# Optimization experiments

Hardware: AMD Instinct MI355X
Metric: run time of the kernel (lower is better)

Reference implementation:

```python
import jax, jax.numpy as jnp
import numpy as np

N, E, B = 10000, 160000, 64
D, ND, ED, L = 640, 4, 8, 6
LN_EPS = 1e-5
COS_EPS = 1e-8


def _conv(x, src, dst, ea, Wq, bq, Wk, bk, Wv, bv, We, Ws, bs):
    # PyG TransformerConv, heads=1, edge features added to key and value.
    n = x.shape[0]
    d = Wq.shape[1]
    q = x @ Wq + bq                      # [N, D]
    k = x @ Wk + bk
    v = x @ Wv + bv
    e = ea @ We                          # [E, D] edge embedding
    ke = k[src] + e                      # [E, D]
    ve = v[src] + e
    score = jnp.sum(q[dst] * ke, axis=-1) * (1.0 / np.sqrt(d).astype(np.float32))
    smax = jax.lax.stop_gradient(jax.ops.segment_max(score, dst, num_segments=n))
    p = jnp.exp(score - smax[dst])
    denom = jax.ops.segment_sum(p, dst, num_segments=n)
    alpha = p / (denom[dst] + 1e-16)     # segment softmax over incoming edges
    agg = jax.ops.segment_sum(ve * alpha[:, None], dst, num_segments=n)
    return agg + x @ Ws + bs             # root/skip connection


def _graph_embed(x, ei, ea, batch, W0q, b0q, W0k, b0k, W0v, b0v, W0e, W0s, b0s,
                 Wq, bq, Wk, bk, Wv, bv, We, Ws, bs, ln_g, ln_b, Wemb, bemb):
    src, dst = ei[0], ei[1]
    h = jax.nn.relu(_conv(x, src, dst, ea, W0q, b0q, W0k, b0k, W0v, b0v, W0e, W0s, b0s))
    for l in range(L - 1):
        h = _conv(h, src, dst, ea, Wq[l], bq[l], Wk[l], bk[l], Wv[l], bv[l], We[l], Ws[l], bs[l])
        if l < L - 2:
            h = jax.nn.relu(h)
    pooled = jax.ops.segment_sum(h, batch, num_segments=B)   # global_add_pool -> [B, D]
    mu = jnp.mean(pooled, axis=-1, keepdims=True)
    var = jnp.var(pooled, axis=-1, keepdims=True)
    z = (pooled - mu) * jax.lax.rsqrt(var + LN_EPS) * ln_g + ln_b
    return jax.nn.relu(z @ Wemb + bemb)                      # [B, D]


def setup_inputs() -> dict:
    key = jax.random.key(0)
    ks = jax.random.split(key, 32)
    s = 0.05
    inp = {
        'x_i': jax.random.normal(ks[0], (N, ND), jnp.float32),
        'edge_index_i': jax.random.randint(ks[1], (2, E), 0, N, jnp.int64),
        'edge_attr_i': jax.random.normal(ks[2], (E, ED), jnp.float32),
        'batch_i': jnp.sort(jax.random.randint(ks[3], (N,), 0, B, jnp.int64)),
        'x_j': jax.random.normal(ks[4], (N, ND), jnp.float32),
        'edge_index_j': jax.random.randint(ks[5], (2, E), 0, N, jnp.int64),
        'edge_attr_j': jax.random.normal(ks[6], (E, ED), jnp.float32),
        'batch_j': jnp.sort(jax.random.randint(ks[7], (N,), 0, B, jnp.int64)),
        # layer 0 (in=node_dim)
        'W0q': jax.random.normal(ks[8], (ND, D), jnp.float32) * s,
        'b0q': jnp.zeros((D,), jnp.float32),
        'W0k': jax.random.normal(ks[9], (ND, D), jnp.float32) * s,
        'b0k': jnp.zeros((D,), jnp.float32),
        'W0v': jax.random.normal(ks[10], (ND, D), jnp.float32) * s,
        'b0v': jnp.zeros((D,), jnp.float32),
        'W0e': jax.random.normal(ks[11], (ED, D), jnp.float32) * s,
        'W0s': jax.random.normal(ks[12], (ND, D), jnp.float32) * s,
        'b0s': jnp.zeros((D,), jnp.float32),
        # layers 1..L-1 (in=out=D), stacked
        'Wq': jax.random.normal(ks[13], (L - 1, D, D), jnp.float32) * s,
        'bq': jnp.zeros((L - 1, D), jnp.float32),
        'Wk': jax.random.normal(ks[14], (L - 1, D, D), jnp.float32) * s,
        'bk': jnp.zeros((L - 1, D), jnp.float32),
        'Wv': jax.random.normal(ks[15], (L - 1, D, D), jnp.float32) * s,
        'bv': jnp.zeros((L - 1, D), jnp.float32),
        'We': jax.random.normal(ks[16], (L - 1, ED, D), jnp.float32) * s,
        'Ws': jax.random.normal(ks[17], (L - 1, D, D), jnp.float32) * s,
        'bs': jnp.zeros((L - 1, D), jnp.float32),
        # embedding head: LayerNorm + Linear + ReLU
        'ln_g': jnp.ones((D,), jnp.float32),
        'ln_b': jnp.zeros((D,), jnp.float32),
        'Wemb': jax.random.normal(ks[18], (D, D), jnp.float32) * s,
        'bemb': jnp.zeros((D,), jnp.float32),
    }
    return inp


def reference(x_i, edge_index_i, edge_attr_i, batch_i,
              x_j, edge_index_j, edge_attr_j, batch_j,
              W0q, b0q, W0k, b0k, W0v, b0v, W0e, W0s, b0s,
              Wq, bq, Wk, bk, Wv, bv, We, Ws, bs,
              ln_g, ln_b, Wemb, bemb):
    zi = _graph_embed(x_i, edge_index_i, edge_attr_i, batch_i, W0q, b0q, W0k, b0k, W0v, b0v,
                      W0e, W0s, b0s, Wq, bq, Wk, bk, Wv, bv, We, Ws, bs, ln_g, ln_b, Wemb, bemb)
    zj = _graph_embed(x_j, edge_index_j, edge_attr_j, batch_j, W0q, b0q, W0k, b0k, W0v, b0v,
                      W0e, W0s, b0s, Wq, bq, Wk, bk, Wv, bv, We, Ws, bs, ln_g, ln_b, Wemb, bemb)
    ni = jnp.maximum(jnp.linalg.norm(zi, axis=-1), COS_EPS)
    nj = jnp.maximum(jnp.linalg.norm(zj, axis=-1), COS_EPS)
    return jnp.sum(zi * zj, axis=-1) / (ni * nj)   # [B]
```

## Files before the change

kernel.cpp:

```cpp
#include <hip/hip_runtime.h>

#define N_NODES 10000
#define N_EDGES 160000
#define NB 64
#define D 640
#define ND_IN 4
#define ED_IN 8
#define NLAYERS 6
#define M_ROWS (2 * N_NODES)

#define SCORE_SCALE 0.039528470752104741f
#define NEGBIG -3.4e38f

typedef __attribute__((ext_vector_type(4))) float floatx4;
typedef __attribute__((ext_vector_type(2))) float floatx2;

__device__ __forceinline__ unsigned short f2bf(float f) {
  unsigned u = __float_as_uint(f);
  u += 0x7fffu + ((u >> 16) & 1);
  return (unsigned short)(u >> 16);
}
__device__ __forceinline__ float bf2f(unsigned short s) {
  return __uint_as_float((unsigned)s << 16);
}
__device__ __forceinline__ void gload_lds16(const void* g, void* l) {
  __builtin_amdgcn_global_load_lds(
      (const __attribute__((address_space(1))) void*)g,
      (__attribute__((address_space(3))) void*)l, 16, 0, 0);
}
__device__ __forceinline__ float4 cvt4(ushort4 s) {
  return make_float4(bf2f(s.x), bf2f(s.y), bf2f(s.z), bf2f(s.w));
}
__device__ __forceinline__ float4 fp8x4_to_f4(unsigned u) {
  floatx2 lo = __builtin_amdgcn_cvt_pk_f32_fp8((int)u, false);
  floatx2 hi = __builtin_amdgcn_cvt_pk_f32_fp8((int)u, true);
  return make_float4(lo[0], lo[1], hi[0], hi[1]);
}
__device__ __forceinline__ unsigned f4_to_fp8x4(float a, float b, float c, float d) {
  int pk = __builtin_amdgcn_cvt_pk_fp8_f32(a, b, 0, false);
  pk = __builtin_amdgcn_cvt_pk_fp8_f32(c, d, pk, true);
  return (unsigned)pk;
}
__device__ __forceinline__ unsigned char f2fp8(float a) {
  return (unsigned char)(__builtin_amdgcn_cvt_pk_fp8_f32(a, 0.f, 0, false) & 0xFF);
}

__global__ void k_lin4(const float* __restrict__ xI, const float* __restrict__ xJ,
                       const float* __restrict__ Wq, const float* __restrict__ bq,
                       const float* __restrict__ Wk, const float* __restrict__ bk,
                       const float* __restrict__ Wv, const float* __restrict__ bv,
                       const float* __restrict__ Ws, const float* __restrict__ bs,
                       unsigned short* __restrict__ oqb, unsigned char* __restrict__ okv,
                       unsigned short* __restrict__ osb) {
  int t = blockIdx.x * blockDim.x + threadIdx.x;
  if (t >= M_ROWS * D) return;
  int z = blockIdx.z;
  const float* W = (z == 0) ? Wq : (z == 1) ? Wk : (z == 2) ? Wv : Ws;
  const float* b = (z == 0) ? bq : (z == 1) ? bk : (z == 2) ? bv : bs;
  int n = t / D, d = t % D;
  const float* xr = (n < N_NODES) ? xI + (size_t)n * ND_IN
                                  : xJ + (size_t)(n - N_NODES) * ND_IN;
  float acc = b[d];
#pragma unroll
  for (int c = 0; c < ND_IN; ++c) acc += xr[c] * W[c * D + d];
  if (z == 0) oqb[t] = f2bf(acc);
  else if (z == 3) osb[t] = f2bf(acc);
  else okv[(size_t)(2 * n + (z - 1)) * D + d] = f2fp8(acc);
}

__global__ __launch_bounds__(256) void k_wprep(const float* __restrict__ Wq,
                                               const float* __restrict__ Wk,
                                               const float* __restrict__ Wv,
                                               const float* __restrict__ Ws,
                                               unsigned char* __restrict__ Wt8) {
  __shared__ float tile[32][33];
  int mt = blockIdx.z;
  int l = mt >> 2, mat = mt & 3;
  const float* W =
      (mat == 0 ? Wq : mat == 1 ? Wk : mat == 2 ? Wv : Ws) + (size_t)l * D * D;
  int tk = blockIdx.x * 32, tn = blockIdx.y * 32;
  int tx = threadIdx.x & 31, ty = threadIdx.x >> 5;
#pragma unroll
  for (int i = 0; i < 32; i += 8)
    tile[ty + i][tx] = W[(size_t)(tk + ty + i) * D + tn + tx];
  __syncthreads();
  unsigned char* dst = Wt8 + (size_t)mt * D * D;
#pragma unroll
  for (int i = 0; i < 32; i += 8)
    dst[(size_t)(tn + ty + i) * D + tk + tx] = f2fp8(tile[tx][ty + i]);
}

#define BM 128
#define BN 128
#define BKF 128
#define RBANDS ((M_ROWS + BM - 1) / BM)
__global__ __launch_bounds__(256) void k_gemm_fp8(
    const unsigned char* __restrict__ Af8, const unsigned char* __restrict__ Wt8,
    const float* __restrict__ b0, const float* __restrict__ b1,
    const float* __restrict__ b2, const float* __restrict__ b3,
    unsigned short* __restrict__ oqb, unsigned char* __restrict__ okv,
    unsigned short* __restrict__ osb) {
  __shared__ __attribute__((aligned(16))) unsigned char lA[BM * BKF];
  __shared__ __attribute__((aligned(16))) unsigned char lB[BN * BKF];
  const int f = blockIdx.x;
  const int xcd = f & 7;
  const int slot = f >> 3;
  const int grp = slot / 20;
  const int tt = slot - grp * 20;
  const int r = xcd + (grp << 3);
  if (r >= RBANDS) return;
  const int z = tt / 5;
  const int by = tt - z * 5;
  const unsigned char* Wz = Wt8 + (size_t)z * D * D;
  const float* bias = (z == 0) ? b0 : (z == 1) ? b1 : (z == 2) ? b2 : b3;
  const int bm = r * BM, bn = by * BN;
  const int t = threadIdx.x;
  const int lane = t & 63, wv = t >> 6;
  const int wm = (wv & 1) * 64, wn = (wv >> 1) * 64;
  const int l15 = lane & 15, l4 = lane >> 4;
  const int srow = lane >> 3;
  const int scb = lane & 7;

  floatx4 acc[4][4] = {};

  for (int k0 = 0; k0 < D; k0 += BKF) {
#pragma unroll
    for (int i = 0; i < 4; ++i) {
      int row = wv * 32 + i * 8 + srow;
      int lcb = scb ^ (row & 7);
      gload_lds16(Af8 + (size_t)(bm + row) * D + k0 + lcb * 16,
                  lA + (size_t)(wv * 32 + i * 8) * BKF);
      gload_lds16(Wz + (size_t)(bn + row) * D + k0 + lcb * 16,
                  lB + (size_t)(wv * 32 + i * 8) * BKF);
    }
    __syncthreads();
#pragma unroll
    for (int kk = 0; kk < 4; ++kk) {
      long af[4], bfr[4];
      int c8 = kk * 4 + l4;
      int blk = c8 >> 1, sub = (c8 & 1) * 8;
#pragma unroll
      for (int i = 0; i < 4; ++i) {
        int rowA = wm + i * 16 + l15;
        af[i] = *(const long*)(lA + (size_t)rowA * BKF +
                               (blk ^ (rowA & 7)) * 16 + sub);
        int rowB = wn + i * 16 + l15;
        bfr[i] = *(const long*)(lB + (size_t)rowB * BKF +
                                (blk ^ (rowB & 7)) * 16 + sub);
      }
#pragma unroll
      for (int ni = 0; ni < 4; ++ni)
#pragma unroll
        for (int mi = 0; mi < 4; ++mi)
          acc[ni][mi] = __builtin_amdgcn_mfma_f32_16x16x32_fp8_fp8(
              bfr[ni], af[mi], acc[ni][mi], 0, 0, 0);
    }
    __syncthreads();
  }
  float4 bia[4];
#pragma unroll
  for (int ni = 0; ni < 4; ++ni)
    bia[ni] = *(const float4*)(bias + bn + wn + ni * 16 + l4 * 4);
#pragma unroll
  for (int mi = 0; mi < 4; ++mi) {
    int row = bm + wm + mi * 16 + l15;
    if (row >= M_ROWS) continue;
#pragma unroll
    for (int ni = 0; ni < 4; ++ni) {
      int col = bn + wn + ni * 16 + l4 * 4;
      float v0 = acc[ni][mi][0] + bia[ni].x;
      float v1 = acc[ni][mi][1] + bia[ni].y;
      float v2 = acc[ni][mi][2] + bia[ni].z;
      float v3 = acc[ni][mi][3] + bia[ni].w;
      if (z == 0 || z == 3) {
        ushort4 pk;
        pk.x = f2bf(v0);
        pk.y = f2bf(v1);
        pk.z = f2bf(v2);
        pk.w = f2bf(v3);
        unsigned short* dst = (z == 0) ? oqb : osb;
        *(ushort4*)(dst + (size_t)row * D + col) = pk;
      } else {
        unsigned pk8 = f4_to_fp8x4(v0, v1, v2, v3);
        *(unsigned*)(okv + (size_t)(2 * row + (z - 1)) * D + col) = pk8;
      }
    }
  }
}

__global__ void k_hist(const int* __restrict__ dstI, const int* __restrict__ dstJ,
                       int* __restrict__ cnt) {
  int e = blockIdx.x * blockDim.x + threadIdx.x;
  if (e >= 2 * N_EDGES) return;
  int d = (e < N_EDGES) ? dstI[e] : (dstJ[e - N_EDGES] + N_NODES);
  atomicAdd(&cnt[d], 1);
}

__global__ __launch_bounds__(1024) void k_scan(const int* __restrict__ cnt,
                                               int* __restrict__ start,
                                               int* __restrict__ cursor) {
  __shared__ int sh[1024];
  __shared__ int carry_sh;
  int tid = threadIdx.x;
  if (tid == 0) {
    carry_sh = 0;
    start[0] = 0;
  }
  __syncthreads();
  for (int base = 0; base < M_ROWS; base += 1024) {
    int idx = base + tid;
    int v = (idx < M_ROWS) ? cnt[idx] : 0;
    sh[tid] = v;
    __syncthreads();
    for (int off = 1; off < 1024; off <<= 1) {
      int t = (tid >= off) ? sh[tid - off] : 0;
      __syncthreads();
      sh[tid] += t;
      __syncthreads();
    }
    int incl = sh[tid] + carry_sh;
    if (idx < M_ROWS) {
      start[idx + 1] = incl;
      cursor[idx] = incl - v;
    }
    __syncthreads();
    if (tid == 1023) carry_sh = incl;
    __syncthreads();
  }
}

__global__ void k_scatter(const int* __restrict__ srcI, const int* __restrict__ dstI,
                          const int* __restrict__ srcJ, const int* __restrict__ dstJ,
                          const float* __restrict__ eaI, const float* __restrict__ eaJ,
                          int* __restrict__ cursor, int* __restrict__ srcS,
                          float* __restrict__ eaS) {
  int e = blockIdx.x * blockDim.x + threadIdx.x;
  if (e >= 2 * N_EDGES) return;
  int s, d;
  const float* eap;
  if (e < N_EDGES) {
    s = srcI[e];
    d = dstI[e];
    eap = eaI + (size_t)e * ED_IN;
  } else {
    s = srcJ[e - N_EDGES] + N_NODES;
    d = dstJ[e - N_EDGES] + N_NODES;
    eap = eaJ + (size_t)(e - N_EDGES) * ED_IN;
  }
  int pos = atomicAdd(&cursor[d], 1);
  srcS[pos] = s;
  float4 a0 = *(const float4*)eap;
  float4 a1 = *(const float4*)(eap + 4);
  *(float4*)(eaS + (size_t)pos * ED_IN) = a0;
  *(float4*)(eaS + (size_t)pos * ED_IN + 4) = a1;
}

__global__ __launch_bounds__(256) void k_edge_fused(
    unsigned char* __restrict__ hf8, unsigned short* __restrict__ hbf,
    const unsigned short* __restrict__ sbf, const unsigned short* __restrict__ qb16,
    const unsigned char* __restrict__ kvf8, const float* __restrict__ eaS,
    const float* __restrict__ We, const int* __restrict__ srcS,
    const int* __restrict__ start, int do_relu, int write_bf) {
  int w = blockIdx.x * 4 + (threadIdx.x >> 6);
  if (w >= M_ROWS) return;
  int l64 = threadIdx.x & 63;
  int g = l64 >> 5, lane = l64 & 31;
  const int s0 = start[w], s1 = start[w + 1];
  const int deg = s1 - s0;
  const int EMAX = 2 * N_EDGES - 1;

  float4 qr[5];
#pragma unroll
  for (int i = 0; i < 5; ++i)
    qr[i] = cvt4(*(const ushort4*)(qb16 + (size_t)w * D + i * 128 + 4 * lane));

  float Gc = 0.f;
#pragma unroll
  for (int c = 0; c < ED_IN; ++c) {
    const float* wr = We + c * D;
    float p = 0.f;
#pragma unroll
    for (int i = 0; i < 5; ++i) {
      float4 wv = *(const float4*)(wr + i * 128 + 4 * lane);
      p += qr[i].x * wv.x + qr[i].y * wv.y + qr[i].z * wv.z + qr[i].w * wv.w;
    }
#pragma unroll
    for (int m = 1; m < 32; m <<= 1) p += __shfl_xor(p, m, 32);
    if (lane == c) Gc = p;
  }

  float mx = NEGBIG, Sp = 0.f, Sea = 0.f;
  float4 acc[5];
#pragma unroll
  for (int i = 0; i < 5; ++i) acc[i] = make_float4(0.f, 0.f, 0.f, 0.f);

  int p0 = s0 + g, p1 = p0 + 2;
  int c0 = min(p0, EMAX), c1 = min(p1, EMAX);
  int sj0 = srcS[c0], sj1 = srcS[c1];
  const int U = (deg + 3) >> 2;
  for (int u = 0; u < U; ++u) {
    bool ok0 = p0 < s1, ok1 = p1 < s1;
    int cc0 = c0, cc1 = c1;
    int tj0 = sj0, tj1 = sj1;
    p0 += 4;
    p1 += 4;
    c0 = min(p0, EMAX);
    c1 = min(p1, EMAX);
    sj0 = srcS[c0];
    sj1 = srcS[c1];

    const unsigned char* r0 = kvf8 + (size_t)tj0 * 2 * D;
    const unsigned char* r1 = kvf8 + (size_t)tj1 * 2 * D;
    float part0 = 0.f, part1 = 0.f;
    float4 vv0[5], vv1[5];
#pragma unroll
    for (int i = 0; i < 5; ++i) {
      int off = i * 128 + 4 * lane;
      float4 k0 = fp8x4_to_f4(*(const unsigned*)(r0 + off));
      float4 k1 = fp8x4_to_f4(*(const unsigned*)(r1 + off));
      vv0[i] = fp8x4_to_f4(*(const unsigned*)(r0 + D + off));
      vv1[i] = fp8x4_to_f4(*(const unsigned*)(r1 + D + off));
      part0 += qr[i].x * k0.x + qr[i].y * k0.y + qr[i].z * k0.z + qr[i].w * k0.w;
      part1 += qr[i].x * k1.x + qr[i].y * k1.y + qr[i].z * k1.z + qr[i].w * k1.w;
    }
    float ea0 = (lane < ED_IN) ? eaS[(size_t)cc0 * ED_IN + lane] : 0.f;
    float ea1 = (lane < ED_IN) ? eaS[(size_t)cc1 * ED_IN + lane] : 0.f;
    part0 += ea0 * Gc;
    part1 += ea1 * Gc;
#pragma unroll
    for (int m = 1; m < 32; m <<= 1) {
      part0 += __shfl_xor(part0, m, 32);
      part1 += __shfl_xor(part1, m, 32);
    }
    float sc0 = ok0 ? part0 * SCORE_SCALE : NEGBIG;
    float sc1 = ok1 ? part1 * SCORE_SCALE : NEGBIG;
    float m2 = fmaxf(sc0, sc1);
    if (m2 > mx) {
      float cs = __expf(mx - m2);
      float pA = __expf(sc0 - m2);
      float pB = __expf(sc1 - m2);
      mx = m2;
      Sp = Sp * cs + pA + pB;
      Sea = Sea * cs + pA * ea0 + pB * ea1;
#pragma unroll
      for (int i = 0; i < 5; ++i) {
        acc[i].x = acc[i].x * cs + pA * vv0[i].x + pB * vv1[i].x;
        acc[i].y = acc[i].y * cs + pA * vv0[i].y + pB * vv1[i].y;
        acc[i].z = acc[i].z * cs + pA * vv0[i].z + pB * vv1[i].z;
        acc[i].w = acc[i].w * cs + pA * vv0[i].w + pB * vv1[i].w;
      }
    } else {
      float pA = __expf(sc0 - mx);
      float pB = __expf(sc1 - mx);
      Sp += pA + pB;
      Sea += pA * ea0 + pB * ea1;
#pragma unroll
      for (int i = 0; i < 5; ++i) {
        acc[i].x += pA * vv0[i].x + pB * vv1[i].x;
        acc[i].y += pA * vv0[i].y + pB * vv1[i].y;
        acc[i].z += pA * vv0[i].z + pB * vv1[i].z;
        acc[i].w += pA * vv0[i].w + pB * vv1[i].w;
      }
    }
  }

  float mo = __shfl_xor(mx, 32);
  float mn = fmaxf(mx, mo);
  float a = __expf(mx - mn);
  float b = __expf(mo - mn);
  float Spo = __shfl_xor(Sp, 32);
  Sp = Sp * a + Spo * b;
  float Seao = __shfl_xor(Sea, 32);
  Sea = Sea * a + Seao * b;
#pragma unroll
  for (int i = 0; i < 5; ++i) {
    float ox = __shfl_xor(acc[i].x, 32);
    float oy = __shfl_xor(acc[i].y, 32);
    float oz = __shfl_xor(acc[i].z, 32);
    float ow = __shfl_xor(acc[i].w, 32);
    acc[i].x = acc[i].x * a + ox * b;
    acc[i].y = acc[i].y * a + oy * b;
    acc[i].z = acc[i].z * a + oz * b;
    acc[i].w = acc[i].w * a + ow * b;
  }
  float inv = 1.0f / (Sp + 1e-16f);
  float seac[ED_IN];
#pragma unroll
  for (int c = 0; c < ED_IN; ++c) seac[c] = __shfl(Sea, c, 32);

  for (int i = g; i < 5; i += 2) {
    int d = i * 128 + 4 * lane;
    float4 term = acc[i];
#pragma unroll
    for (int c = 0; c < ED_IN; ++c) {
      float4 wv = *(const float4*)(We + c * D + d);
      term.x += seac[c] * wv.x;
      term.y += seac[c] * wv.y;
      term.z += seac[c] * wv.z;
      term.w += seac[c] * wv.w;
    }
    ushort4 sv = *(const ushort4*)(sbf + (size_t)w * D + d);
    float vx = bf2f(sv.x) + term.x * inv;
    float vy = bf2f(sv.y) + term.y * inv;
    float vz = bf2f(sv.z) + term.z * inv;
    float vw = bf2f(sv.w) + term.w * inv;
    if (do_relu) {
      vx = fmaxf(vx, 0.f);
      vy = fmaxf(vy, 0.f);
      vz = fmaxf(vz, 0.f);
      vw = fmaxf(vw, 0.f);
    }
    if (write_bf) {
      ushort4 hb;
      hb.x = f2bf(vx);
      hb.y = f2bf(vy);
      hb.z = f2bf(vz);
      hb.w = f2bf(vw);
      *(ushort4*)(hbf + (size_t)w * D + d) = hb;
    } else {
      *(unsigned*)(hf8 + (size_t)w * D + d) = f4_to_fp8x4(vx, vy, vz, vw);
    }
  }
}

__global__ void k_ranges(const int* __restrict__ batI, const int* __restrict__ batJ,
                         int* __restrict__ rng) {
  int b = threadIdx.x;
  if (b > 2 * NB) return;
  if (b == 2 * NB) {
    rng[b] = M_ROWS;
    return;
  }
  const int* bat = (b < NB) ? batI : batJ;
  int tgt = (b < NB) ? b : b - NB;
  int lo = 0, hi = N_NODES;
  while (lo < hi) {
    int mid = (lo + hi) >> 1;
    if (bat[mid] < tgt) lo = mid + 1;
    else hi = mid;
  }
  rng[b] = lo + ((b < NB) ? 0 : N_NODES);
}

__global__ __launch_bounds__(256) void k_pool_seg(const unsigned short* __restrict__ hbf,
                                                  const int* __restrict__ rng,
                                                  float* __restrict__ pooled) {
  int b = blockIdx.x;
  int lo = rng[b], hi = rng[b + 1];
  int ch = threadIdx.x;
  if (ch >= 160) return;
  float4 s = make_float4(0.f, 0.f, 0.f, 0.f);
  for (int n = lo; n < hi; ++n) {
    ushort4 v = *(const ushort4*)(hbf + (size_t)n * D + ch * 4);
    s.x += bf2f(v.x);
    s.y += bf2f(v.y);
    s.z += bf2f(v.z);
    s.w += bf2f(v.w);
  }
  *(float4*)(pooled + (size_t)b * D + ch * 4) = s;
}

__global__ __launch_bounds__(256) void k_head(const float* __restrict__ pooled,
                                              const float* __restrict__ gam,
                                              const float* __restrict__ bet,
                                              const float* __restrict__ Wemb,
                                              const float* __restrict__ bemb,
                                              float* __restrict__ z) {
  __shared__ float sh[D];
  __shared__ float red[4];
  int b = blockIdx.x, tid = threadIdx.x;
  float local = 0.f;
  for (int c = tid; c < D; c += 256) {
    float val = pooled[(size_t)b * D + c];
    sh[c] = val;
    local += val;
  }
#pragma unroll
  for (int off = 32; off > 0; off >>= 1) local += __shfl_down(local, off);
  if ((tid & 63) == 0) red[tid >> 6] = local;
  __syncthreads();
  float mu = (red[0] + red[1] + red[2] + red[3]) * (1.0f / D);
  __syncthreads();
  float lv = 0.f;
  for (int c = tid; c < D; c += 256) {
    float t2 = sh[c] - mu;
    lv += t2 * t2;
  }
#pragma unroll
  for (int off = 32; off > 0; off >>= 1) lv += __shfl_down(lv, off);
  if ((tid & 63) == 0) red[tid >> 6] = lv;
  __syncthreads();
  float var = (red[0] + red[1] + red[2] + red[3]) * (1.0f / D);
  float rstd = rsqrtf(var + 1e-5f);
  __syncthreads();
  for (int c = tid; c < D; c += 256) sh[c] = (sh[c] - mu) * rstd * gam[c] + bet[c];
  __syncthreads();
  for (int d = tid; d < D; d += 256) {
    float acc = bemb[d];
    for (int c = 0; c < D; ++c) acc += sh[c] * Wemb[c * D + d];
    z[(size_t)b * D + d] = fmaxf(acc, 0.f);
  }
}

__global__ void k_cosine(const float* __restrict__ zi, const float* __restrict__ zj,
                         float* __restrict__ out) {
  int b = blockIdx.x, lane = threadIdx.x;
  float dot = 0.f, ni = 0.f, nj = 0.f;
  for (int d = lane; d < D; d += 64) {
    float a = zi[(size_t)b * D + d], c = zj[(size_t)b * D + d];
    dot += a * c;
    ni += a * a;
    nj += c * c;
  }
#pragma unroll
  for (int off = 32; off > 0; off >>= 1) {
    dot += __shfl_down(dot, off);
    ni += __shfl_down(ni, off);
    nj += __shfl_down(nj, off);
  }
  if (lane == 0)
    out[b] = dot / (fmaxf(sqrtf(ni), 1e-8f) * fmaxf(sqrtf(nj), 1e-8f));
}

extern "C" void kernel_launch(void* const* d_in, const int* in_sizes, int n_in,
                              void* d_out, int out_size, void* d_ws, size_t ws_size,
                              hipStream_t stream) {
  (void)in_sizes; (void)n_in; (void)out_size; (void)ws_size;
  const float* xI = (const float*)d_in[0];
  const int* eiI = (const int*)d_in[1];
  const float* eaI = (const float*)d_in[2];
  const int* batI = (const int*)d_in[3];
  const float* xJ = (const float*)d_in[4];
  const int* eiJ = (const int*)d_in[5];
  const float* eaJ = (const float*)d_in[6];
  const int* batJ = (const int*)d_in[7];
  const float* W0q = (const float*)d_in[8];
  const float* b0q = (const float*)d_in[9];
  const float* W0k = (const float*)d_in[10];
  const float* b0k = (const float*)d_in[11];
  const float* W0v = (const float*)d_in[12];
  const float* b0v = (const float*)d_in[13];
  const float* W0e = (const float*)d_in[14];
  const float* W0s = (const float*)d_in[15];
  const float* b0s = (const float*)d_in[16];
  const float* Wq = (const float*)d_in[17];
  const float* bq = (const float*)d_in[18];
  const float* Wk = (const float*)d_in[19];
  const float* bk = (const float*)d_in[20];
  const float* Wv = (const float*)d_in[21];
  const float* bv = (const float*)d_in[22];
  const float* We = (const float*)d_in[23];
  const float* Ws = (const float*)d_in[24];
  const float* bs = (const float*)d_in[25];
  const float* ln_g = (const float*)d_in[26];
  const float* ln_b = (const float*)d_in[27];
  const float* Wemb = (const float*)d_in[28];
  const float* bemb = (const float*)d_in[29];

  const size_t ND2 = (size_t)M_ROWS * D;
  float* pooled = (float*)d_ws;
  float* z = pooled + (size_t)2 * NB * D;
  float* eaS = z + (size_t)2 * NB * D;
  unsigned short* qbf = (unsigned short*)(eaS + (size_t)2 * N_EDGES * ED_IN);
  unsigned char* kvf8 = (unsigned char*)(qbf + ND2);
  unsigned char* hf8 = kvf8 + 2 * ND2;
  unsigned short* hbf = (unsigned short*)(hf8 + ND2);
  unsigned short* sbf = hbf + ND2;
  unsigned char* Wt8 = (unsigned char*)(sbf + ND2);
  int* cnt = (int*)(Wt8 + (size_t)(NLAYERS - 1) * 4 * D * D);
  int* start = cnt + M_ROWS;
  int* cursor = start + M_ROWS + 1;
  int* srcS = cursor + M_ROWS;
  int* rng = srcS + 2 * N_EDGES;

  const int* srcI = eiI;
  const int* dstI = eiI + N_EDGES;
  const int* srcJ = eiJ;
  const int* dstJ = eiJ + N_EDGES;

  dim3 gLin4((M_ROWS * D + 255) / 256, 1, 4);
  dim3 gGemm(8 * 20 * 20);
  dim3 gEdge((M_ROWS + 3) / 4);
  dim3 gE((2 * N_EDGES + 255) / 256);

  k_wprep<<<dim3(D / 32, D / 32, (NLAYERS - 1) * 4), 256, 0, stream>>>(Wq, Wk, Wv, Ws, Wt8);

  hipMemsetAsync(cnt, 0, M_ROWS * sizeof(int), stream);
  k_hist<<<gE, 256, 0, stream>>>(dstI, dstJ, cnt);
  k_scan<<<1, 1024, 0, stream>>>(cnt, start, cursor);
  k_scatter<<<gE, 256, 0, stream>>>(srcI, dstI, srcJ, dstJ, eaI, eaJ, cursor,
                                    srcS, eaS);
  k_ranges<<<1, 192, 0, stream>>>(batI, batJ, rng);

  k_lin4<<<gLin4, 256, 0, stream>>>(xI, xJ, W0q, b0q, W0k, b0k, W0v, b0v, W0s,
                                    b0s, qbf, kvf8, sbf);
  k_edge_fused<<<gEdge, 256, 0, stream>>>(hf8, hbf, sbf, qbf, kvf8, eaS, W0e,
                                          srcS, start, 1, 0);

  for (int l = 0; l < NLAYERS - 1; ++l) {
    const unsigned char* WtL = Wt8 + (size_t)l * 4 * D * D;
    const float* Wel = We + (size_t)l * ED_IN * D;
    int last = (l == NLAYERS - 2);
    k_gemm_fp8<<<gGemm, 256, 0, stream>>>(
        hf8, WtL, bq + (size_t)l * D, bk + (size_t)l * D, bv + (size_t)l * D,
        bs + (size_t)l * D, qbf, kvf8, sbf);
    k_edge_fused<<<gEdge, 256, 0, stream>>>(hf8, hbf, sbf, qbf, kvf8, eaS, Wel,
                                            srcS, start, last ? 0 : 1,
                                            last ? 1 : 0);
  }

  k_pool_seg<<<2 * NB, 256, 0, stream>>>(hbf, rng, pooled);
  k_head<<<2 * NB, 256, 0, stream>>>(pooled, ln_g, ln_b, Wemb, bemb, z);
  k_cosine<<<NB, 64, 0, stream>>>(z, z + (size_t)NB * D, (float*)d_out);
}
```

Before: 1.343 ms.

## Enlarge GEMM row tile to 256 with 8 waves; process 4 edges per half-wave in attention

The FP8 GEMM now uses 256-row tiles with 512 threads (8 waves), so each loaded weight tile is reused across twice as many rows and the grid is halved. The edge attention kernel handles four edges per half-wave iteration instead of two, issuing all K/V fp8 loads before the dot products to expose more memory-level parallelism. The edge-feature projection Gc is split across the two half-waves and merged with a shuffle. These changes raise register and LDS pressure per block and lower GEMM block count, which may reduce occupancy.

```diff
diff --git a/kernel.cpp b/kernel.cpp
--- a/kernel.cpp
+++ b/kernel.cpp
@@ -90,11 +90,11 @@
     dst[(size_t)(tn + ty + i) * D + tk + tx] = f2fp8(tile[tx][ty + i]);
 }
 
-#define BM 128
+#define BM 256
 #define BN 128
 #define BKF 128
 #define RBANDS ((M_ROWS + BM - 1) / BM)
-__global__ __launch_bounds__(256) void k_gemm_fp8(
+__global__ __launch_bounds__(512) void k_gemm_fp8(
     const unsigned char* __restrict__ Af8, const unsigned char* __restrict__ Wt8,
     const float* __restrict__ b0, const float* __restrict__ b1,
     const float* __restrict__ b2, const float* __restrict__ b3,
@@ -115,8 +115,8 @@
   const float* bias = (z == 0) ? b0 : (z == 1) ? b1 : (z == 2) ? b2 : b3;
   const int bm = r * BM, bn = by * BN;
   const int t = threadIdx.x;
-  const int lane = t & 63, wv = t >> 6;
-  const int wm = (wv & 1) * 64, wn = (wv >> 1) * 64;
+  const int lane = t & 63, wv8 = t >> 6;
+  const int wm = (wv8 & 3) * 64, wn = (wv8 >> 2) * 64;
   const int l15 = lane & 15, l4 = lane >> 4;
   const int srow = lane >> 3;
   const int scb = lane & 7;
@@ -126,12 +126,17 @@
   for (int k0 = 0; k0 < D; k0 += BKF) {
 #pragma unroll
     for (int i = 0; i < 4; ++i) {
-      int row = wv * 32 + i * 8 + srow;
+      int row = wv8 * 32 + i * 8 + srow;
       int lcb = scb ^ (row & 7);
       gload_lds16(Af8 + (size_t)(bm + row) * D + k0 + lcb * 16,
-                  lA + (size_t)(wv * 32 + i * 8) * BKF);
+                  lA + (size_t)(wv8 * 32 + i * 8) * BKF);
+    }
+#pragma unroll
+    for (int i = 0; i < 2; ++i) {
+      int row = wv8 * 16 + i * 8 + srow;
+      int lcb = scb ^ (row & 7);
       gload_lds16(Wz + (size_t)(bn + row) * D + k0 + lcb * 16,
-                  lB + (size_t)(wv * 32 + i * 8) * BKF);
+                  lB + (size_t)(wv8 * 16 + i * 8) * BKF);
     }
     __syncthreads();
 #pragma unroll
@@ -274,10 +279,10 @@
   for (int i = 0; i < 5; ++i)
     qr[i] = cvt4(*(const ushort4*)(qb16 + (size_t)w * D + i * 128 + 4 * lane));
 
-  float Gc = 0.f;
-#pragma unroll
-  for (int c = 0; c < ED_IN; ++c) {
-    const float* wr = We + c * D;
+  float gv = 0.f;
+#pragma unroll
+  for (int j = 0; j < 4; ++j) {
+    const float* wr = We + (4 * g + j) * D;
     float p = 0.f;
 #pragma unroll
     for (int i = 0; i < 5; ++i) {
@@ -286,7 +291,13 @@
     }
 #pragma unroll
     for (int m = 1; m < 32; m <<= 1) p += __shfl_xor(p, m, 32);
-    if (lane == c) Gc = p;
+    if (lane == j) gv = p;
+  }
+  float Gc = 0.f;
+  {
+    int src = (lane < 4) ? lane : (32 + lane - 4);
+    float tg = __shfl(gv, src, 64);
+    if (lane < ED_IN) Gc = tg;
   }
 
   float mx = NEGBIG, Sp = 0.f, Sea = 0.f;
@@ -294,72 +305,104 @@
 #pragma unroll
   for (int i = 0; i < 5; ++i) acc[i] = make_float4(0.f, 0.f, 0.f, 0.f);
 
-  int p0 = s0 + g, p1 = p0 + 2;
-  int c0 = min(p0, EMAX), c1 = min(p1, EMAX);
-  int sj0 = srcS[c0], sj1 = srcS[c1];
-  const int U = (deg + 3) >> 2;
+  int pos[4], cc[4], sj[4];
+#pragma unroll
+  for (int j = 0; j < 4; ++j) {
+    pos[j] = s0 + g + 2 * j;
+    cc[j] = min(pos[j], EMAX);
+    sj[j] = srcS[cc[j]];
+  }
+  const int U = (deg + 7) >> 3;
   for (int u = 0; u < U; ++u) {
-    bool ok0 = p0 < s1, ok1 = p1 < s1;
-    int cc0 = c0, cc1 = c1;
-    int tj0 = sj0, tj1 = sj1;
-    p0 += 4;
-    p1 += 4;
-    c0 = min(p0, EMAX);
-    c1 = min(p1, EMAX);
-    sj0 = srcS[c0];
-    sj1 = srcS[c1];
-
-    const unsigned char* r0 = kvf8 + (size_t)tj0 * 2 * D;
-    const unsigned char* r1 = kvf8 + (size_t)tj1 * 2 * D;
-    float part0 = 0.f, part1 = 0.f;
-    float4 vv0[5], vv1[5];
-#pragma unroll
-    for (int i = 0; i < 5; ++i) {
-      int off = i * 128 + 4 * lane;
-      float4 k0 = fp8x4_to_f4(*(const unsigned*)(r0 + off));
-      float4 k1 = fp8x4_to_f4(*(const unsigned*)(r1 + off));
-      vv0[i] = fp8x4_to_f4(*(const unsigned*)(r0 + D + off));
-      vv1[i] = fp8x4_to_f4(*(const unsigned*)(r1 + D + off));
-      part0 += qr[i].x * k0.x + qr[i].y * k0.y + qr[i].z * k0.z + qr[i].w * k0.w;
-      part1 += qr[i].x * k1.x + qr[i].y * k1.y + qr[i].z * k1.z + qr[i].w * k1.w;
-    }
-    float ea0 = (lane < ED_IN) ? eaS[(size_t)cc0 * ED_IN + lane] : 0.f;
-    float ea1 = (lane < ED_IN) ? eaS[(size_t)cc1 * ED_IN + lane] : 0.f;
-    part0 += ea0 * Gc;
-    part1 += ea1 * Gc;
+    bool ok[4];
+    int tcc[4], tsj[4];
+#pragma unroll
+    for (int j = 0; j < 4; ++j) {
+      ok[j] = pos[j] < s1;
+      tcc[j] = cc[j];
+      tsj[j] = sj[j];
+      pos[j] += 8;
+      cc[j] = min(pos[j], EMAX);
+      sj[j] = srcS[cc[j]];
+    }
+    unsigned kp[4][5], vp[4][5];
+#pragma unroll
+    for (int j = 0; j < 4; ++j) {
+      const unsigned char* r = kvf8 + (size_t)tsj[j] * 2 * D;
+#pragma unroll
+      for (int i = 0; i < 5; ++i) {
+        int off = i * 128 + 4 * lane;
+        kp[j][i] = *(const unsigned*)(r + off);
+        vp[j][i] = *(const unsigned*)(r + D + off);
+      }
+    }
+    float ea[4];
+#pragma unroll
+    for (int j = 0; j < 4; ++j)
+      ea[j] = (lane < ED_IN) ? eaS[(size_t)tcc[j] * ED_IN + lane] : 0.f;
+    float part[4];
+#pragma unroll
+    for (int j = 0; j < 4; ++j) {
+      float s = 0.f;
+#pragma unroll
+      for (int i = 0; i < 5; ++i) {
+        float4 kv = fp8x4_to_f4(kp[j][i]);
+        s += qr[i].x * kv.x + qr[i].y * kv.y + qr[i].z * kv.z + qr[i].w * kv.w;
+      }
+      part[j] = s + ea[j] * Gc;
+    }
 #pragma unroll
     for (int m = 1; m < 32; m <<= 1) {
-      part0 += __shfl_xor(part0, m, 32);
-      part1 += __shfl_xor(part1, m, 32);
-    }
-    float sc0 = ok0 ? part0 * SCORE_SCALE : NEGBIG;
-    float sc1 = ok1 ? part1 * SCORE_SCALE : NEGBIG;
-    float m2 = fmaxf(sc0, sc1);
-    if (m2 > mx) {
-      float cs = __expf(mx - m2);
-      float pA = __expf(sc0 - m2);
-      float pB = __expf(sc1 - m2);
-      mx = m2;
-      Sp = Sp * cs + pA + pB;
-      Sea = Sea * cs + pA * ea0 + pB * ea1;
+#pragma unroll
+      for (int j = 0; j < 4; ++j) part[j] += __shfl_xor(part[j], m, 32);
+    }
+    float sc[4];
+#pragma unroll
+    for (int j = 0; j < 4; ++j)
+      sc[j] = ok[j] ? part[j] * SCORE_SCALE : NEGBIG;
+    float m4 = fmaxf(fmaxf(sc[0], sc[1]), fmaxf(sc[2], sc[3]));
+    float p[4];
+    if (m4 > mx) {
+      float cs = __expf(mx - m4);
+      mx = m4;
+#pragma unroll
+      for (int j = 0; j < 4; ++j) p[j] = __expf(sc[j] - m4);
+      Sp = Sp * cs + p[0] + p[1] + p[2] + p[3];
+      Sea = Sea * cs + p[0] * ea[0] + p[1] * ea[1] + p[2] * ea[2] + p[3] * ea[3];
 #pragma unroll
       for (int i = 0; i < 5; ++i) {
-        acc[i].x = acc[i].x * cs + pA * vv0[i].x + pB * vv1[i].x;
-        acc[i].y = acc[i].y * cs + pA * vv0[i].y + pB * vv1[i].y;
-        acc[i].z = acc[i].z * cs + pA * vv0[i].z + pB * vv1[i].z;
-        acc[i].w = acc[i].w * cs + pA * vv0[i].w + pB * vv1[i].w;
+        float4 a = acc[i];
+        a.x *= cs;
+        a.y *= cs;
+        a.z *= cs;
+        a.w *= cs;
+#pragma unroll
+        for (int j = 0; j < 4; ++j) {
+          float4 v = fp8x4_to_f4(vp[j][i]);
+          a.x += p[j] * v.x;
+          a.y += p[j] * v.y;
+          a.z += p[j] * v.z;
+          a.w += p[j] * v.w;
+        }
+        acc[i] = a;
       }
     } else {
-      float pA = __expf(sc0 - mx);
-      float pB = __expf(sc1 - mx);
-      Sp += pA + pB;
-      Sea += pA * ea0 + pB * ea1;
+#pragma unroll
+      for (int j = 0; j < 4; ++j) p[j] = __expf(sc[j] - mx);
+      Sp += p[0] + p[1] + p[2] + p[3];
+      Sea += p[0] * ea[0] + p[1] * ea[1] + p[2] * ea[2] + p[3] * ea[3];
 #pragma unroll
       for (int i = 0; i < 5; ++i) {
-        acc[i].x += pA * vv0[i].x + pB * vv1[i].x;
-        acc[i].y += pA * vv0[i].y + pB * vv1[i].y;
-        acc[i].z += pA * vv0[i].z + pB * vv1[i].z;
-        acc[i].w += pA * vv0[i].w + pB * vv1[i].w;
+        float4 a = acc[i];
+#pragma unroll
+        for (int j = 0; j < 4; ++j) {
+          float4 v = fp8x4_to_f4(vp[j][i]);
+          a.x += p[j] * v.x;
+          a.y += p[j] * v.y;
+          a.z += p[j] * v.z;
+          a.w += p[j] * v.w;
+        }
+        acc[i] = a;
       }
     }
   }
@@ -579,7 +622,7 @@
   const int* dstJ = eiJ + N_EDGES;
 
   dim3 gLin4((M_ROWS * D + 255) / 256, 1, 4);
-  dim3 gGemm(8 * 20 * 20);
+  dim3 gGemm(8 * 10 * 20);
   dim3 gEdge((M_ROWS + 3) / 4);
   dim3 gE((2 * N_EDGES + 255) / 256);
 
@@ -601,7 +644,7 @@
     const unsigned char* WtL = Wt8 + (size_t)l * 4 * D * D;
     const float* Wel = We + (size_t)l * ED_IN * D;
     int last = (l == NLAYERS - 2);
-    k_gemm_fp8<<<gGemm, 256, 0, stream>>>(
+    k_gemm_fp8<<<gGemm, 512, 0, stream>>>(
         hf8, WtL, bq + (size_t)l * D, bk + (size_t)l * D, bv + (size_t)l * D,
         bs + (size_t)l * D, qbf, kvf8, sbf);
     k_edge_fused<<<gEdge, 256, 0, stream>>>(hf8, hbf, sbf, qbf, kvf8, eaS, Wel,
```

After: 1.663 ms. +23.8%, slower.
